# Kernel tuning notes

Measured on AMD Instinct MI355X. Metric: run time of the kernel, lower is better.

## Reference

```python
import jax, jax.numpy as jnp
import numpy as np

D = 200      # embedding_dim
R = 460      # 2 * num_rel
T = 32       # num_t (timestamps)
B = 2048     # batch of queries
NUM_E = 10000


def _gru(x, h, W_ih, W_hh, b_ih, b_hh):
    # torch.nn.GRUCell semantics
    gi = x @ W_ih.T + b_ih
    gh = h @ W_hh.T + b_hh
    ir, iz, inn = jnp.split(gi, 3, axis=-1)
    hr, hz, hn = jnp.split(gh, 3, axis=-1)
    r = jax.nn.sigmoid(ir + hr)
    z = jax.nn.sigmoid(iz + hz)
    n = jnp.tanh(inn + r * hn)
    return (1.0 - z) * n + z * h


def _mk_linear(k, out_dim, in_dim):
    kw, kb = jax.random.split(k)
    bound = 1.0 / np.sqrt(in_dim)
    W = jax.random.uniform(kw, (out_dim, in_dim), minval=-bound, maxval=bound, dtype=jnp.float32)
    b = jax.random.uniform(kb, (out_dim,), minval=-bound, maxval=bound, dtype=jnp.float32)
    return W, b


def setup_inputs():
    key = jax.random.key(0)
    ks = jax.random.split(key, 20)
    pre_emb = jax.random.normal(ks[0], (NUM_E, D), dtype=jnp.float32) * 0.05
    r_emb = jax.random.normal(ks[1], (R, D), dtype=jnp.float32) * 0.05
    sub = jax.random.randint(ks[2], (B,), 0, NUM_E)
    rel = jax.random.randint(ks[3], (B,), 0, R)
    obj = jax.random.randint(ks[4], (B,), 0, NUM_E)
    all_triples = jnp.stack([sub, rel, obj], axis=1)
    mask = jax.random.bernoulli(ks[5], 0.1, (B, T * R))
    partial_embeding = jax.random.uniform(ks[6], (B, T * R), dtype=jnp.float32) * mask
    cur_ts = jax.random.randint(ks[7], (B,), 0, T)
    W_map1, b_map1 = _mk_linear(ks[8], 2 * D, D)
    W_map2, b_map2 = _mk_linear(ks[9], D, 2 * D)
    W_attn, b_attn = _mk_linear(ks[10], D, D)
    W_ih, b_ih = _mk_linear(ks[11], 3 * D, D)
    W_hh, b_hh = _mk_linear(ks[12], 3 * D, D)
    W_h1, b_h1 = _mk_linear(ks[13], D, D)
    W_h2, b_h2 = _mk_linear(ks[14], D, D)
    W_align, b_align = _mk_linear(ks[15], D, D)
    return {
        'pre_emb': pre_emb, 'r_emb': r_emb, 'all_triples': all_triples,
        'partial_embeding': partial_embeding, 'cur_ts': cur_ts,
        'W_map1': W_map1, 'b_map1': b_map1, 'W_map2': W_map2, 'b_map2': b_map2,
        'W_attn': W_attn, 'b_attn': b_attn,
        'W_ih': W_ih, 'W_hh': W_hh, 'b_ih': b_ih, 'b_hh': b_hh,
        'W_h1': W_h1, 'b_h1': b_h1, 'W_h2': W_h2, 'b_h2': b_h2,
        'W_align': W_align, 'b_align': b_align,
    }


def reference(pre_emb, r_emb, all_triples, partial_embeding, cur_ts,
              W_map1, b_map1, W_map2, b_map2, W_attn, b_attn,
              W_ih, W_hh, b_ih, b_hh, W_h1, b_h1, W_h2, b_h2,
              W_align, b_align):
    # rel_mapping2(rel_mapping1(r_emb)) -> [R, D]
    mapped_rel = (r_emb @ W_map1.T + b_map1) @ W_map2.T + b_map2
    q_rel = mapped_rel[all_triples[:, 1]]                      # [B, D]
    # attention logits base is constant over timesteps: linear_attn(q_rel) @ mapped_rel^T
    base = (q_rel @ W_attn.T + b_attn) @ mapped_rel.T          # [B, R]
    part = partial_embeding.reshape(B, T, R).transpose(1, 0, 2)  # [T, B, R]
    ts = jnp.arange(T)

    # The torch code sorts by cur_ts and runs GRU steps for ts in [0, cur_ts_j) per sample.
    # Equivalent fully-batched form: scan over T, freeze hidden once t >= cur_ts_j.
    def step(h, inp):
        t, cur = inp                                           # cur: [B, R]
        attn = cur * base
        attn = jnp.where(attn == 0, jnp.float32(-1e9), attn)
        a = jax.nn.softmax(attn, axis=1)
        x = a @ mapped_rel                                     # [B, D]
        h_new = _gru(x, h, W_ih, W_hh, b_ih, b_hh)
        h = jnp.where((t < cur_ts)[:, None], h_new, h)
        return h, None

    h0 = jnp.zeros((B, D), dtype=jnp.float32)
    gru_hidden_all, _ = jax.lax.scan(step, h0, (ts, part))

    # predicted_hist = 0.1 * rel2hist2(rel2hist(q_rel)) + q_rel
    predicted_hist = 0.1 * ((q_rel @ W_h1.T + b_h1) @ W_h2.T + b_h2) + q_rel
    match_loss = jnp.mean((predicted_hist - gru_hidden_all) ** 2)

    # forward_forth with distmult scoring
    gh = _gru(q_rel, predicted_hist, W_ih, W_hh, b_ih, b_hh)
    sub_emb = pre_emb[all_triples[:, 0]]
    aligned_all = pre_emb @ W_align.T + b_align                # [NUM_E, D]
    aligned_sub = sub_emb @ W_align.T + b_align                # [B, D]
    score_ = (aligned_sub * gh) @ aligned_all.T                # [B, NUM_E]
    labels = jax.nn.one_hot(all_triples[:, 2], NUM_E, dtype=jnp.float32)
    # BCELoss(sigmoid(score_), labels), stably via log-sigmoid
    path_loss = -jnp.mean(labels * jax.nn.log_sigmoid(score_)
                          + (1.0 - labels) * jax.nn.log_sigmoid(-score_))
    score = jax.nn.sigmoid(score_)
    return match_loss, path_loss, score
```

## Files before the change

### kernel.cpp

```cpp
#include <hip/hip_runtime.h>
#include <cstdint>
#include <cstddef>

typedef unsigned short u16;
typedef __attribute__((ext_vector_type(8))) short short8;
typedef __attribute__((ext_vector_type(4))) float f32x4;

__device__ __forceinline__ f32x4 mfma16(short8 a, short8 b, f32x4 c){
  return __builtin_amdgcn_mfma_f32_16x16x32_bf16(a, b, c, 0, 0, 0);
}
__device__ __forceinline__ float bf2f(u16 u){
  unsigned v = ((unsigned)u) << 16; float f; __builtin_memcpy(&f, &v, 4); return f;
}
__device__ __forceinline__ u16 f2bf(float f){
  unsigned u; __builtin_memcpy(&u, &f, 4);
  u += 0x7FFFu + ((u >> 16) & 1u);
  return (u16)(u >> 16);
}
__device__ __forceinline__ float sigf(float x){ return 1.f / (1.f + __expf(-x)); }

struct CvtD { const float* s; u16* d; int M, K, Mp, Kp; };
struct CvtTab { CvtD t[10]; };

__global__ void cvt_all(CvtTab tab){
  CvtD de = tab.t[blockIdx.y];
  int total = de.Mp * de.Kp;
  for (int i = blockIdx.x * blockDim.x + threadIdx.x; i < total; i += gridDim.x * blockDim.x){
    int r = i / de.Kp, c = i - r * de.Kp;
    float v = (r < de.M && c < de.K) ? de.s[(size_t)r * de.K + c] : 0.f;
    de.d[i] = f2bf(v);
  }
}

__global__ void gather_qrel(const u16* __restrict__ mbf, const float* __restrict__ m32,
                            const int* __restrict__ trip, u16* __restrict__ qbf,
                            float* __restrict__ q32){
  int i = blockIdx.x * blockDim.x + threadIdx.x;
  if (i < 2048 * 256){
    int b = i >> 8, c = i & 255;
    int rel = trip[b * 3 + 1];
    qbf[i] = mbf[rel * 256 + c];
    if (c < 200) q32[b * 200 + c] = m32[rel * 200 + c];
  }
}

__global__ void cntt_k(const int* __restrict__ cur_ts, int* __restrict__ cntt,
                       float* __restrict__ out0){
  int t = blockIdx.x;
  __shared__ int psum[256];
  int tid = threadIdx.x, s = 0;
  #pragma unroll
  for (int k = 0; k < 8; ++k) s += (cur_ts[tid * 8 + k] > t) ? 1 : 0;
  psum[tid] = s; __syncthreads();
  for (int st = 128; st > 0; st >>= 1){
    if (tid < st) psum[tid] += psum[tid + st];
    __syncthreads();
  }
  if (tid == 0){
    cntt[t] = psum[0];
    if (t == 0){ out0[0] = 0.f; out0[1] = 0.f; }
  }
}
__global__ void toff_k(const int* __restrict__ cntt, int* __restrict__ toff){
  if (threadIdx.x == 0){
    int run = 0;
    for (int t = 0; t < 32; ++t){ toff[t] = run; run += cntt[t]; }
    toff[32] = run;
  }
}
__global__ void fill_pairs_t(const int* __restrict__ cur_ts, const int* __restrict__ toff,
                             int* __restrict__ pairs){
  int t = blockIdx.x;
  __shared__ int psum[256];
  int tid = threadIdx.x;
  int loc[8]; int tsum = 0;
  #pragma unroll
  for (int k = 0; k < 8; ++k){ loc[k] = (cur_ts[tid * 8 + k] > t) ? 1 : 0; tsum += loc[k]; }
  psum[tid] = tsum; __syncthreads();
  for (int st = 1; st < 256; st <<= 1){
    int v = (tid >= st) ? psum[tid - st] : 0;
    __syncthreads();
    psum[tid] += v;
    __syncthreads();
  }
  int run = psum[tid] - tsum + toff[t];
  #pragma unroll
  for (int k = 0; k < 8; ++k)
    if (loc[k]){ pairs[run] = t * 2048 + tid * 8 + k; ++run; }
}

template<int MODE, int GROUP>
__global__ __launch_bounds__(256) void gemm_bt(
    const u16* A, int lda,
    const u16* B, int ldb,
    int K, int Mreal, int Nreal,
    const float* bias,
    float* C32,
    u16* C16, int ldc16,
    const float* __restrict__ extra,
    const float* __restrict__ extra2,
    const int* __restrict__ trip,
    float* __restrict__ loss,
    const int* __restrict__ tcnt,
    const u16* A2, const u16* B2, const float* bias2, float* C32b, u16* C16b,
    int Mreal2, int ldc16b)
{
  __shared__ u16 AB[3][2][128 * 32];
  __shared__ float red[256];
  const int tid = threadIdx.x;
  const int wave = tid >> 6, lane = tid & 63;

  if (MODE == 0 && blockIdx.z){
    A = A2; B = B2; bias = bias2; C32 = C32b; C16 = C16b;
    Mreal = Mreal2; ldc16 = ldc16b;
  }

  const int gx = gridDim.x, gy = gridDim.y;
  const int nwg = gx * gy;
  int orig = blockIdx.y * gx + blockIdx.x;
  int q = nwg >> 3, r8 = nwg & 7;
  int xcd = orig & 7, idx = orig >> 3;
  int fid = (xcd < r8 ? xcd * (q + 1) : r8 * (q + 1) + (xcd - r8) * q) + idx;
  int mx, my;
  if (GROUP == 0){ my = fid / gx; mx = fid - my * gx; }
  else           { mx = fid / gy; my = fid - mx * gy; }

  const int m0 = my * 128, n0 = mx * 128;

  int Mg_ = Mreal;
  if (MODE == 3) Mg_ = tcnt[32];
  if (m0 >= Mg_) return;

  const int wm = (wave >> 1) * 64, wn = (wave & 1) * 64;
  const int srow = lane >> 2;
  const int scol = (((lane & 3) ^ (srow & 3)) * 8);
  const int fr = lane & 15, fkg = lane >> 4;
  const int slot = (fkg ^ (fr & 3)) * 8;

  f32x4 acc[4][4];
  #pragma unroll
  for (int i = 0; i < 4; ++i)
    #pragma unroll
    for (int j = 0; j < 4; ++j) acc[i][j] = (f32x4){0.f, 0.f, 0.f, 0.f};

  const int kT = (K + 31) >> 5;

  auto STAGE = [&](int kt, int p){
    #pragma unroll
    for (int i = 0; i < 2; ++i){
      int ch = wave * 2 + i;
      const u16* ga = A + (size_t)(m0 + ch * 16 + srow) * lda + kt * 32 + scol;
      __builtin_amdgcn_global_load_lds((const __attribute__((address_space(1))) void*)ga,
          (__attribute__((address_space(3))) void*)(&AB[p][0][0] + ch * 512), 16, 0, 0);
      const u16* gb = B + (size_t)(n0 + ch * 16 + srow) * ldb + kt * 32 + scol;
      __builtin_amdgcn_global_load_lds((const __attribute__((address_space(1))) void*)gb,
          (__attribute__((address_space(3))) void*)(&AB[p][1][0] + ch * 512), 16, 0, 0);
    }
  };

  STAGE(0, 0);
  if (kT > 1) STAGE(1, 1);
  for (int kt = 0; kt < kT; ++kt){
    const int p = kt % 3;
    if (kt + 1 < kT){
      __builtin_amdgcn_sched_barrier(0);
      asm volatile("s_waitcnt vmcnt(4)" ::: "memory");
    } else {
      __builtin_amdgcn_sched_barrier(0);
      asm volatile("s_waitcnt vmcnt(0)" ::: "memory");
    }
    __builtin_amdgcn_sched_barrier(0);
    __builtin_amdgcn_s_barrier();
    __builtin_amdgcn_sched_barrier(0);

    if (kt + 2 < kT) STAGE(kt + 2, (kt + 2) % 3);

    short8 av[4], bv[4];
    #pragma unroll
    for (int i = 0; i < 4; ++i){
      av[i] = *(const short8*)(&AB[p][0][0] + (wm + i * 16 + fr) * 32 + slot);
      bv[i] = *(const short8*)(&AB[p][1][0] + (wn + i * 16 + fr) * 32 + slot);
    }
    #pragma unroll
    for (int i = 0; i < 4; ++i)
      #pragma unroll
      for (int j = 0; j < 4; ++j)
        acc[i][j] = mfma16(av[i], bv[j], acc[i][j]);
  }

  if (MODE == 2){
    float lsum = 0.f;
    #pragma unroll
    for (int i = 0; i < 4; ++i){
      #pragma unroll
      for (int r = 0; r < 4; ++r){
        int row = m0 + wm + i * 16 + (lane >> 4) * 4 + r;
        int tcol = trip[row * 3 + 2];
        #pragma unroll
        for (int j = 0; j < 4; ++j){
          int col = n0 + wn + j * 16 + fr;
          if (col < Nreal){
            float v = acc[i][j][r];
            float e = __expf(-fabsf(v));
            float inv = __builtin_amdgcn_rcpf(1.f + e);
            C32[2 + (size_t)row * Nreal + col] = (v >= 0.f) ? inv : e * inv;
            float x = (tcol == col) ? v : -v;
            lsum += fminf(x, 0.f) - __logf(1.f + e);
          }
        }
      }
    }
    red[tid] = lsum;
    __syncthreads();
    for (int s = 128; s > 0; s >>= 1){
      if (tid < s) red[tid] += red[tid + s];
      __syncthreads();
    }
    if (tid == 0) atomicAdd(loss, -red[0] * (1.f / 20480000.f));
    return;
  }

  if (MODE == 3){
    #pragma unroll
    for (int i = 0; i < 4; ++i){
      #pragma unroll
      for (int r = 0; r < 4; ++r){
        int row = m0 + wm + i * 16 + (lane >> 4) * 4 + r;
        if (row < Mg_){
          int orow = trip[row];
          #pragma unroll
          for (int j = 0; j < 4; ++j){
            int col = n0 + wn + j * 16 + fr;
            if (col < Nreal)
              C16[(size_t)orow * ldc16 + col] = f2bf(acc[i][j][r] + bias[col]);
          }
        }
      }
    }
    return;
  }

  if (MODE == 1){
    float lsum = 0.f;
    #pragma unroll
    for (int i = 0; i < 4; ++i){
      #pragma unroll
      for (int j = 0; j < 4; ++j){
        int col = n0 + wn + j * 16 + fr;
        float bvl = (col < Nreal) ? bias[col] : 0.f;
        #pragma unroll
        for (int r = 0; r < 4; ++r){
          int row = m0 + wm + i * 16 + (lane >> 4) * 4 + r;
          if (col < Nreal){
            float pv = 0.1f * (acc[i][j][r] + bvl) + extra[(size_t)row * Nreal + col];
            C32[(size_t)row * Nreal + col] = pv;
            C16[(size_t)row * ldc16 + col] = f2bf(pv);
            float d = pv - extra2[(size_t)row * Nreal + col];
            lsum += d * d;
          } else {
            C16[(size_t)row * ldc16 + col] = 0;
          }
        }
      }
    }
    red[tid] = lsum;
    __syncthreads();
    for (int s = 128; s > 0; s >>= 1){
      if (tid < s) red[tid] += red[tid + s];
      __syncthreads();
    }
    if (tid == 0) atomicAdd(loss, red[0] * (1.f / 409600.f));
    return;
  }

  #pragma unroll
  for (int i = 0; i < 4; ++i){
    #pragma unroll
    for (int j = 0; j < 4; ++j){
      int col = n0 + wn + j * 16 + fr;
      float bvl = 0.f;
      if (bias && col < Nreal) bvl = bias[col];
      #pragma unroll
      for (int r = 0; r < 4; ++r){
        int row = m0 + wm + i * 16 + (lane >> 4) * 4 + r;
        float v = acc[i][j][r] + bvl;
        if (C32 && row < Mreal && col < Nreal) C32[(size_t)row * Nreal + col] = v;
        if (C16) C16[(size_t)row * ldc16 + col] =
            (row < Mreal && col < Nreal) ? f2bf(v) : (u16)0;
      }
    }
  }
}

__global__ __launch_bounds__(256) void softmax_c(
    const float* __restrict__ part, const float* __restrict__ base,
    const int* __restrict__ pairs, const int* __restrict__ toff,
    u16* __restrict__ aout)
{
  int wave = threadIdx.x >> 6, lane = threadIdx.x & 63;
  int hi = toff[32];
  for (int j = blockIdx.x * 4 + wave; j < hi; j += gridDim.x * 4){
    int p = pairs[j];
    int b = p & 2047, t = p >> 11;
    const float* pr = part + (size_t)b * 14720 + t * 460;
    const float* br = base + (size_t)b * 460;
    int r0 = lane * 8;
    float vals[8];
    if (lane < 57){
      float4 pa = *(const float4*)(pr + r0);
      float4 pb = *(const float4*)(pr + r0 + 4);
      float4 ba = *(const float4*)(br + r0);
      float4 bb = *(const float4*)(br + r0 + 4);
      float pv[8] = {pa.x, pa.y, pa.z, pa.w, pb.x, pb.y, pb.z, pb.w};
      float bw[8] = {ba.x, ba.y, ba.z, ba.w, bb.x, bb.y, bb.z, bb.w};
      #pragma unroll
      for (int u = 0; u < 8; ++u){
        float a = pv[u] * bw[u];
        bool valid = (r0 + u) < 460;
        vals[u] = (!valid) ? -__builtin_inff() : ((a == 0.f) ? -1000000000.0f : a);
      }
    } else {
      #pragma unroll
      for (int u = 0; u < 8; ++u){
        int r = r0 + u;
        if (r < 460){
          float a = pr[r] * br[r];
          vals[u] = (a == 0.f) ? -1000000000.0f : a;
        } else vals[u] = -__builtin_inff();
      }
    }
    float m = vals[0];
    #pragma unroll
    for (int u = 1; u < 8; ++u) m = fmaxf(m, vals[u]);
    #pragma unroll
    for (int s = 1; s < 64; s <<= 1) m = fmaxf(m, __shfl_xor(m, s));
    float e[8]; float sum = 0.f;
    #pragma unroll
    for (int u = 0; u < 8; ++u){
      float x = vals[u];
      float ev = (x == -__builtin_inff()) ? 0.f : __expf(x - m);
      e[u] = ev; sum += ev;
    }
    #pragma unroll
    for (int s = 1; s < 64; s <<= 1) sum += __shfl_xor(sum, s);
    float inv = __builtin_amdgcn_rcpf(sum);
    union { u16 o[8]; uint4 v; } pk;
    #pragma unroll
    for (int u = 0; u < 8; ++u) pk.o[u] = f2bf(e[u] * inv);
    *(uint4*)(aout + (size_t)j * 512 + r0) = pk.v;
  }
}

__global__ __launch_bounds__(512, 2) void gru_scan3(
    const u16* __restrict__ gi_all,
    const u16* __restrict__ Whh,
    const float* __restrict__ bhh,
    const int* __restrict__ cur_ts,
    float* __restrict__ hout)
{
  __shared__ u16 hbf[16 * 256];
  __shared__ float hf[8 * 200];
  __shared__ float ghs[8][648];
  __shared__ u16 gis[2][8 * 640];
  __shared__ float bhs[600];
  __shared__ int cts[8];
  const int tid = threadIdx.x, wave = tid >> 6, lane = tid & 63;
  const int rb = blockIdx.x * 8;
  const int fr = lane & 15, fkg = lane >> 4;
  const int fk = fkg * 8;

  for (int i = tid; i < 16 * 256; i += 512) hbf[i] = 0;
  for (int i = tid; i < 8 * 200; i += 512) hf[i] = 0.f;
  for (int i = tid; i < 600; i += 512) bhs[i] = bhh[i];
  if (tid < 8) cts[tid] = cur_ts[rb + tid];
  __syncthreads();
  int Trun = 0;
  #pragma unroll
  for (int r = 0; r < 8; ++r) Trun = max(Trun, cts[r]);

  short8 wb[5][7];
  #pragma unroll
  for (int f = 0; f < 5; ++f)
    #pragma unroll
    for (int ks = 0; ks < 7; ++ks)
      wb[f][ks] = *(const short8*)(Whh + (size_t)(wave * 80 + f * 16 + fr) * 256 + ks * 32 + fk);

  if (Trun > 0){
    const u16* src = gi_all + (size_t)rb * 640;
    __builtin_amdgcn_global_load_lds(
        (const __attribute__((address_space(1))) void*)(src + tid * 8),
        (__attribute__((address_space(3))) void*)(&gis[0][0] + tid * 8), 16, 0, 0);
    if (tid < 128)
      __builtin_amdgcn_global_load_lds(
          (const __attribute__((address_space(1))) void*)(src + (512 + tid) * 8),
          (__attribute__((address_space(3))) void*)(&gis[0][0] + (512 + tid) * 8), 16, 0, 0);
  }
  __syncthreads();

  const int grow = wave;
  const int crow = (Trun > 0) ? cts[grow] : 0;

  for (int t = 0; t < Trun; ++t){
    f32x4 acc[5];
    #pragma unroll
    for (int f = 0; f < 5; ++f) acc[f] = (f32x4){0.f, 0.f, 0.f, 0.f};
    #pragma unroll
    for (int ks = 0; ks < 7; ++ks){
      short8 av = *(const short8*)(hbf + ((fr * 256 + ks * 32 + fk) ^ ((fr & 7) << 3)));
      #pragma unroll
      for (int f = 0; f < 5; ++f)
        acc[f] = mfma16(av, wb[f][ks], acc[f]);
    }
    if (fkg < 2){
      #pragma unroll
      for (int f = 0; f < 5; ++f){
        int col = wave * 80 + f * 16 + fr;
        #pragma unroll
        for (int r = 0; r < 4; ++r)
          ghs[fkg * 4 + r][col] = acc[f][r];
      }
    }
    __builtin_amdgcn_sched_barrier(0);
    asm volatile("s_waitcnt vmcnt(0) lgkmcnt(0)" ::: "memory");
    __builtin_amdgcn_sched_barrier(0);
    __builtin_amdgcn_s_barrier();
    __builtin_amdgcn_sched_barrier(0);

    if (t + 1 < Trun){
      const u16* src = gi_all + ((size_t)(t + 1) * 2048 + rb) * 640;
      u16* dst = &gis[(t + 1) & 1][0];
      __builtin_amdgcn_global_load_lds(
          (const __attribute__((address_space(1))) void*)(src + tid * 8),
          (__attribute__((address_space(3))) void*)(dst + tid * 8), 16, 0, 0);
      if (tid < 128)
        __builtin_amdgcn_global_load_lds(
            (const __attribute__((address_space(1))) void*)(src + (512 + tid) * 8),
            (__attribute__((address_space(3))) void*)(dst + (512 + tid) * 8), 16, 0, 0);
    }

    if (t < crow){
      const u16* gr = &gis[t & 1][0] + grow * 640;
      #pragma unroll
      for (int k = 0; k < 4; ++k){
        int d = lane + 64 * k;
        if (d < 200){
          float i0 = bf2f(gr[d]);
          float i1 = bf2f(gr[200 + d]);
          float i2 = bf2f(gr[400 + d]);
          float g0 = ghs[grow][d] + bhs[d];
          float g1 = ghs[grow][200 + d] + bhs[200 + d];
          float g2 = ghs[grow][400 + d] + bhs[400 + d];
          float e0 = __expf(-(i0 + g0));
          float r_ = __builtin_amdgcn_rcpf(1.f + e0);
          float e1 = __expf(-(i1 + g1));
          float z  = __builtin_amdgcn_rcpf(1.f + e1);
          float xn = i2 + r_ * g2;
          float e2 = __expf(2.f * xn);
          float n_ = 1.f - 2.f * __builtin_amdgcn_rcpf(e2 + 1.f);
          float hn = (1.f - z) * n_ + z * hf[grow * 200 + d];
          hf[grow * 200 + d] = hn;
          hbf[(grow * 256 + d) ^ (grow << 3)] = f2bf(hn);
        }
      }
    }
    __builtin_amdgcn_sched_barrier(0);
    asm volatile("s_waitcnt lgkmcnt(0)" ::: "memory");
    __builtin_amdgcn_sched_barrier(0);
    __builtin_amdgcn_s_barrier();
    __builtin_amdgcn_sched_barrier(0);
  }

  for (int i = tid; i < 1600; i += 512){
    int row = i / 200, d = i - row * 200;
    hout[(size_t)(rb + row) * 200 + d] = hf[row * 200 + d];
  }
}

__global__ __launch_bounds__(256) void gru2_abig(const float* __restrict__ gi,
                                                 const float* __restrict__ gg,
                                                 const float* __restrict__ hprev,
                                                 const float* __restrict__ al32,
                                                 const int* __restrict__ trip,
                                                 u16* __restrict__ abig){
  int i = blockIdx.x * 256 + threadIdx.x;
  if (i < 2048 * 256){
    int b = i >> 8, c = i & 255;
    u16 v = 0;
    if (c < 200){
      float i0 = gi[b * 600 + c], i1 = gi[b * 600 + 200 + c], i2 = gi[b * 600 + 400 + c];
      float g0 = gg[b * 600 + c], g1 = gg[b * 600 + 200 + c], g2 = gg[b * 600 + 400 + c];
      float r = sigf(i0 + g0);
      float z = sigf(i1 + g1);
      float n = tanhf(i2 + r * g2);
      float gh = (1.f - z) * n + z * hprev[b * 200 + c];
      int sub = trip[b * 3 + 0];
      v = f2bf(al32[(size_t)sub * 200 + c] * gh);
    }
    abig[i] = v;
  }
}

extern "C" void kernel_launch(void* const* d_in, const int* in_sizes, int n_in,
                              void* d_out, int out_size, void* d_ws, size_t ws_size,
                              hipStream_t stream)
{
  (void)in_sizes; (void)n_in; (void)out_size; (void)ws_size;
  const float* pre_emb = (const float*)d_in[0];
  const float* r_emb   = (const float*)d_in[1];
  const int*   trip    = (const int*)d_in[2];
  const float* part    = (const float*)d_in[3];
  const int*   cur_ts  = (const int*)d_in[4];
  const float* Wmap1 = (const float*)d_in[5];   const float* bmap1 = (const float*)d_in[6];
  const float* Wmap2 = (const float*)d_in[7];   const float* bmap2 = (const float*)d_in[8];
  const float* Wattn = (const float*)d_in[9];   const float* battn = (const float*)d_in[10];
  const float* Wih   = (const float*)d_in[11];  const float* Whh   = (const float*)d_in[12];
  const float* bih   = (const float*)d_in[13];  const float* bhh   = (const float*)d_in[14];
  const float* Wh1   = (const float*)d_in[15];  const float* bh1   = (const float*)d_in[16];
  const float* Wh2   = (const float*)d_in[17];  const float* bh2   = (const float*)d_in[18];
  const float* Wal   = (const float*)d_in[19];  const float* bal   = (const float*)d_in[20];
  float* out = (float*)d_out;

  char* wsb = (char*)d_ws;
  size_t off = 0;
  auto alloc = [&](size_t bytes) -> void* {
    void* p = wsb + off;
    off = (off + bytes + 255) & ~(size_t)255;
    return p;
  };
  u16* re_bf     = (u16*)alloc((size_t)512 * 256 * 2);
  u16* wmap1_bf  = (u16*)alloc((size_t)512 * 256 * 2);
  u16* wmap2_bf  = (u16*)alloc((size_t)256 * 448 * 2);
  u16* wattn_bf  = (u16*)alloc((size_t)256 * 256 * 2);
  u16* wih_bf    = (u16*)alloc((size_t)640 * 256 * 2);
  u16* whh_bf    = (u16*)alloc((size_t)640 * 256 * 2);
  u16* wh1_bf    = (u16*)alloc((size_t)256 * 256 * 2);
  u16* wh2_bf    = (u16*)alloc((size_t)256 * 256 * 2);
  u16* wal_bf    = (u16*)alloc((size_t)256 * 256 * 2);
  u16* pre_bf    = (u16*)alloc((size_t)10112 * 256 * 2);
  u16* hidden_bf = (u16*)alloc((size_t)512 * 512 * 2);
  u16* mrel_bf   = (u16*)alloc((size_t)512 * 256 * 2);
  u16* m2t_bf    = (u16*)alloc((size_t)640 * 512 * 2);
  u16* qrel_bf   = (u16*)alloc((size_t)2048 * 256 * 2);
  u16* qa_bf     = (u16*)alloc((size_t)2048 * 256 * 2);
  u16* ph1_bf    = (u16*)alloc((size_t)2048 * 256 * 2);
  u16* ph_bf     = (u16*)alloc((size_t)2048 * 256 * 2);
  u16* abig_bf   = (u16*)alloc((size_t)2048 * 256 * 2);
  u16* gi_all    = (u16*)alloc((size_t)65536 * 640 * 2);
  float* mrel32 = (float*)alloc((size_t)460 * 200 * 4);
  float* base32 = (float*)alloc((size_t)2048 * 460 * 4);
  float* qrel32 = (float*)alloc((size_t)2048 * 200 * 4);
  float* hout   = (float*)alloc((size_t)2048 * 200 * 4);
  float* ph32   = (float*)alloc((size_t)2048 * 200 * 4);
  int* pairs    = (int*)alloc((size_t)65536 * 4);
  int* cntt     = (int*)alloc((size_t)64 * 4);
  int* toff     = (int*)alloc((size_t)64 * 4);
  char* U = (char*)alloc((size_t)40000 * 512 * 2);
  u16*   a_comp = (u16*)U;
  float* gi2    = (float*)(U);
  float* ghg    = (float*)(U + (size_t)5  * 1024 * 1024);
  float* al32   = (float*)(U + (size_t)12 * 1024 * 1024);
  u16*   al_bf  = (u16*)  (U + (size_t)21 * 1024 * 1024);

  cntt_k<<<32, 256, 0, stream>>>(cur_ts, cntt, out);
  toff_k<<<1, 32, 0, stream>>>(cntt, toff);
  fill_pairs_t<<<32, 256, 0, stream>>>(cur_ts, toff, pairs);

  CvtTab tab;
  tab.t[0] = { r_emb,   re_bf,    460, 200,   512, 256 };
  tab.t[1] = { Wmap1,   wmap1_bf, 400, 200,   512, 256 };
  tab.t[2] = { Wmap2,   wmap2_bf, 200, 400,   256, 448 };
  tab.t[3] = { Wattn,   wattn_bf, 200, 200,   256, 256 };
  tab.t[4] = { Wih,     wih_bf,   600, 200,   640, 256 };
  tab.t[5] = { Whh,     whh_bf,   600, 200,   640, 256 };
  tab.t[6] = { Wh1,     wh1_bf,   200, 200,   256, 256 };
  tab.t[7] = { Wh2,     wh2_bf,   200, 200,   256, 256 };
  tab.t[8] = { Wal,     wal_bf,   200, 200,   256, 256 };
  tab.t[9] = { pre_emb, pre_bf, 10000, 200, 10112, 256 };
  cvt_all<<<dim3(512, 10), 256, 0, stream>>>(tab);

  gemm_bt<0,0><<<dim3(4, 4), 256, 0, stream>>>(re_bf, 256, wmap1_bf, 256, 200, 460, 400,
      bmap1, nullptr, hidden_bf, 512, nullptr, nullptr, nullptr, nullptr, nullptr,
      nullptr, nullptr, nullptr, nullptr, nullptr, 0, 0);
  gemm_bt<0,0><<<dim3(2, 4), 256, 0, stream>>>(hidden_bf, 512, wmap2_bf, 448, 400, 460, 200,
      bmap2, mrel32, mrel_bf, 256, nullptr, nullptr, nullptr, nullptr, nullptr,
      nullptr, nullptr, nullptr, nullptr, nullptr, 0, 0);
  gather_qrel<<<2048, 256, 0, stream>>>(mrel_bf, mrel32, trip, qrel_bf, qrel32);

  gemm_bt<0,0><<<dim3(2, 16, 2), 256, 0, stream>>>(qrel_bf, 256, wattn_bf, 256, 200, 2048, 200,
      battn, nullptr, qa_bf, 256, nullptr, nullptr, nullptr, nullptr, nullptr,
      qrel_bf, wh1_bf, bh1, nullptr, ph1_bf, 2048, 256);

  gemm_bt<0,0><<<dim3(4, 16, 2), 256, 0, stream>>>(qa_bf, 256, mrel_bf, 256, 200, 2048, 460,
      nullptr, base32, nullptr, 0, nullptr, nullptr, nullptr, nullptr, nullptr,
      wih_bf, mrel_bf, nullptr, nullptr, m2t_bf, 600, 512);

  softmax_c<<<2048, 256, 0, stream>>>(part, base32, pairs, toff, a_comp);
  gemm_bt<3,0><<<dim3(5, 313), 256, 0, stream>>>(a_comp, 512, m2t_bf, 512, 460, 0, 600,
      bih, nullptr, gi_all, 640, nullptr, nullptr, pairs, nullptr, toff,
      nullptr, nullptr, nullptr, nullptr, nullptr, 0, 0);

  gru_scan3<<<256, 512, 0, stream>>>(gi_all, whh_bf, bhh, cur_ts, hout);

  gemm_bt<1,0><<<dim3(2, 16), 256, 0, stream>>>(ph1_bf, 256, wh2_bf, 256, 200, 2048, 200,
      bh2, ph32, ph_bf, 256, qrel32, hout, nullptr, out, nullptr,
      nullptr, nullptr, nullptr, nullptr, nullptr, 0, 0);

  gemm_bt<0,0><<<dim3(5, 16, 2), 256, 0, stream>>>(qrel_bf, 256, wih_bf, 256, 200, 2048, 600,
      bih, gi2, nullptr, 0, nullptr, nullptr, nullptr, nullptr, nullptr,
      ph_bf, whh_bf, bhh, ghg, nullptr, 2048, 0);

  gemm_bt<0,0><<<dim3(2, 79), 256, 0, stream>>>(pre_bf, 256, wal_bf, 256, 200, 10000, 200,
      bal, al32, al_bf, 256, nullptr, nullptr, nullptr, nullptr, nullptr,
      nullptr, nullptr, nullptr, nullptr, nullptr, 0, 0);

  gru2_abig<<<2048, 256, 0, stream>>>(gi2, ghg, ph32, al32, trip, abig_bf);

  gemm_bt<2,1><<<dim3(79, 16), 256, 0, stream>>>(abig_bf, 256, al_bf, 256, 200, 2048, 10000,
      nullptr, out, nullptr, 0, nullptr, nullptr, trip, out + 1, nullptr,
      nullptr, nullptr, nullptr, nullptr, nullptr, 0, 0);
}
```

Before: 341.2 us.

## Replace LDS-staged GEMM pipeline with direct global fragment loads and compile-time K

The GEMM kernel no longer stages A/B tiles through shared memory with a triple-buffered global_load_lds pipeline and barriers. Each wave now loads its MFMA fragments straight from global memory, and the K-tile count becomes a template parameter so the loop fully unrolls. This removes barrier and LDS traffic for these small-K GEMMs, but each wave re-reads data that other waves also fetch and relies on cache for reuse. The scratch buffer is enlarged slightly, likely to cover reads past row ends.

```diff
diff --git a/kernel.cpp b/kernel.cpp
--- a/kernel.cpp
+++ b/kernel.cpp
@@ -89,7 +89,7 @@
     if (loc[k]){ pairs[run] = t * 2048 + tid * 8 + k; ++run; }
 }
 
-template<int MODE, int GROUP>
+template<int MODE, int GROUP, int KT>
 __global__ __launch_bounds__(256) void gemm_bt(
     const u16* A, int lda,
     const u16* B, int ldb,
@@ -105,7 +105,6 @@
     const u16* A2, const u16* B2, const float* bias2, float* C32b, u16* C16b,
     int Mreal2, int ldc16b)
 {
-  __shared__ u16 AB[3][2][128 * 32];
   __shared__ float red[256];
   const int tid = threadIdx.x;
   const int wave = tid >> 6, lane = tid & 63;
@@ -132,10 +131,10 @@
   if (m0 >= Mg_) return;
 
   const int wm = (wave >> 1) * 64, wn = (wave & 1) * 64;
-  const int srow = lane >> 2;
-  const int scol = (((lane & 3) ^ (srow & 3)) * 8);
   const int fr = lane & 15, fkg = lane >> 4;
-  const int slot = (fkg ^ (fr & 3)) * 8;
+
+  const u16* Ab = A + (size_t)(m0 + wm + fr) * lda + fkg * 8;
+  const u16* Bb = B + (size_t)(n0 + wn + fr) * ldb + fkg * 8;
 
   f32x4 acc[4][4];
   #pragma unroll
@@ -143,43 +142,13 @@
     #pragma unroll
     for (int j = 0; j < 4; ++j) acc[i][j] = (f32x4){0.f, 0.f, 0.f, 0.f};
 
-  const int kT = (K + 31) >> 5;
-
-  auto STAGE = [&](int kt, int p){
-    #pragma unroll
-    for (int i = 0; i < 2; ++i){
-      int ch = wave * 2 + i;
-      const u16* ga = A + (size_t)(m0 + ch * 16 + srow) * lda + kt * 32 + scol;
-      __builtin_amdgcn_global_load_lds((const __attribute__((address_space(1))) void*)ga,
-          (__attribute__((address_space(3))) void*)(&AB[p][0][0] + ch * 512), 16, 0, 0);
-      const u16* gb = B + (size_t)(n0 + ch * 16 + srow) * ldb + kt * 32 + scol;
-      __builtin_amdgcn_global_load_lds((const __attribute__((address_space(1))) void*)gb,
-          (__attribute__((address_space(3))) void*)(&AB[p][1][0] + ch * 512), 16, 0, 0);
-    }
-  };
-
-  STAGE(0, 0);
-  if (kT > 1) STAGE(1, 1);
-  for (int kt = 0; kt < kT; ++kt){
-    const int p = kt % 3;
-    if (kt + 1 < kT){
-      __builtin_amdgcn_sched_barrier(0);
-      asm volatile("s_waitcnt vmcnt(4)" ::: "memory");
-    } else {
-      __builtin_amdgcn_sched_barrier(0);
-      asm volatile("s_waitcnt vmcnt(0)" ::: "memory");
-    }
-    __builtin_amdgcn_sched_barrier(0);
-    __builtin_amdgcn_s_barrier();
-    __builtin_amdgcn_sched_barrier(0);
-
-    if (kt + 2 < kT) STAGE(kt + 2, (kt + 2) % 3);
-
+  #pragma unroll
+  for (int kt = 0; kt < KT; ++kt){
     short8 av[4], bv[4];
     #pragma unroll
     for (int i = 0; i < 4; ++i){
-      av[i] = *(const short8*)(&AB[p][0][0] + (wm + i * 16 + fr) * 32 + slot);
-      bv[i] = *(const short8*)(&AB[p][1][0] + (wn + i * 16 + fr) * 32 + slot);
+      av[i] = *(const short8*)(Ab + (size_t)(i * 16) * lda + kt * 32);
+      bv[i] = *(const short8*)(Bb + (size_t)(i * 16) * ldb + kt * 32);
     }
     #pragma unroll
     for (int i = 0; i < 4; ++i)
@@ -554,7 +523,7 @@
   int* pairs    = (int*)alloc((size_t)65536 * 4);
   int* cntt     = (int*)alloc((size_t)64 * 4);
   int* toff     = (int*)alloc((size_t)64 * 4);
-  char* U = (char*)alloc((size_t)40000 * 512 * 2);
+  char* U = (char*)alloc((size_t)40200 * 512 * 2);
   u16*   a_comp = (u16*)U;
   float* gi2    = (float*)(U);
   float* ghg    = (float*)(U + (size_t)5  * 1024 * 1024);
@@ -578,44 +547,44 @@
   tab.t[9] = { pre_emb, pre_bf, 10000, 200, 10112, 256 };
   cvt_all<<<dim3(512, 10), 256, 0, stream>>>(tab);
 
-  gemm_bt<0,0><<<dim3(4, 4), 256, 0, stream>>>(re_bf, 256, wmap1_bf, 256, 200, 460, 400,
+  gemm_bt<0,0,7><<<dim3(4, 4), 256, 0, stream>>>(re_bf, 256, wmap1_bf, 256, 200, 460, 400,
       bmap1, nullptr, hidden_bf, 512, nullptr, nullptr, nullptr, nullptr, nullptr,
       nullptr, nullptr, nullptr, nullptr, nullptr, 0, 0);
-  gemm_bt<0,0><<<dim3(2, 4), 256, 0, stream>>>(hidden_bf, 512, wmap2_bf, 448, 400, 460, 200,
+  gemm_bt<0,0,13><<<dim3(2, 4), 256, 0, stream>>>(hidden_bf, 512, wmap2_bf, 448, 400, 460, 200,
       bmap2, mrel32, mrel_bf, 256, nullptr, nullptr, nullptr, nullptr, nullptr,
       nullptr, nullptr, nullptr, nullptr, nullptr, 0, 0);
   gather_qrel<<<2048, 256, 0, stream>>>(mrel_bf, mrel32, trip, qrel_bf, qrel32);
 
-  gemm_bt<0,0><<<dim3(2, 16, 2), 256, 0, stream>>>(qrel_bf, 256, wattn_bf, 256, 200, 2048, 200,
+  gemm_bt<0,0,7><<<dim3(2, 16, 2), 256, 0, stream>>>(qrel_bf, 256, wattn_bf, 256, 200, 2048, 200,
       battn, nullptr, qa_bf, 256, nullptr, nullptr, nullptr, nullptr, nullptr,
       qrel_bf, wh1_bf, bh1, nullptr, ph1_bf, 2048, 256);
 
-  gemm_bt<0,0><<<dim3(4, 16, 2), 256, 0, stream>>>(qa_bf, 256, mrel_bf, 256, 200, 2048, 460,
+  gemm_bt<0,0,7><<<dim3(4, 16, 2), 256, 0, stream>>>(qa_bf, 256, mrel_bf, 256, 200, 2048, 460,
       nullptr, base32, nullptr, 0, nullptr, nullptr, nullptr, nullptr, nullptr,
       wih_bf, mrel_bf, nullptr, nullptr, m2t_bf, 600, 512);
 
   softmax_c<<<2048, 256, 0, stream>>>(part, base32, pairs, toff, a_comp);
-  gemm_bt<3,0><<<dim3(5, 313), 256, 0, stream>>>(a_comp, 512, m2t_bf, 512, 460, 0, 600,
+  gemm_bt<3,0,15><<<dim3(5, 313), 256, 0, stream>>>(a_comp, 512, m2t_bf, 512, 460, 0, 600,
       bih, nullptr, gi_all, 640, nullptr, nullptr, pairs, nullptr, toff,
       nullptr, nullptr, nullptr, nullptr, nullptr, 0, 0);
 
   gru_scan3<<<256, 512, 0, stream>>>(gi_all, whh_bf, bhh, cur_ts, hout);
 
-  gemm_bt<1,0><<<dim3(2, 16), 256, 0, stream>>>(ph1_bf, 256, wh2_bf, 256, 200, 2048, 200,
+  gemm_bt<1,0,7><<<dim3(2, 16), 256, 0, stream>>>(ph1_bf, 256, wh2_bf, 256, 200, 2048, 200,
       bh2, ph32, ph_bf, 256, qrel32, hout, nullptr, out, nullptr,
       nullptr, nullptr, nullptr, nullptr, nullptr, 0, 0);
 
-  gemm_bt<0,0><<<dim3(5, 16, 2), 256, 0, stream>>>(qrel_bf, 256, wih_bf, 256, 200, 2048, 600,
+  gemm_bt<0,0,7><<<dim3(5, 16, 2), 256, 0, stream>>>(qrel_bf, 256, wih_bf, 256, 200, 2048, 600,
       bih, gi2, nullptr, 0, nullptr, nullptr, nullptr, nullptr, nullptr,
       ph_bf, whh_bf, bhh, ghg, nullptr, 2048, 0);
 
-  gemm_bt<0,0><<<dim3(2, 79), 256, 0, stream>>>(pre_bf, 256, wal_bf, 256, 200, 10000, 200,
+  gemm_bt<0,0,7><<<dim3(2, 79), 256, 0, stream>>>(pre_bf, 256, wal_bf, 256, 200, 10000, 200,
       bal, al32, al_bf, 256, nullptr, nullptr, nullptr, nullptr, nullptr,
       nullptr, nullptr, nullptr, nullptr, nullptr, 0, 0);
 
   gru2_abig<<<2048, 256, 0, stream>>>(gi2, ghg, ph32, al32, trip, abig_bf);
 
-  gemm_bt<2,1><<<dim3(79, 16), 256, 0, stream>>>(abig_bf, 256, al_bf, 256, 200, 2048, 10000,
+  gemm_bt<2,1,7><<<dim3(79, 16), 256, 0, stream>>>(abig_bf, 256, al_bf, 256, 200, 2048, 10000,
       nullptr, out, nullptr, 0, nullptr, nullptr, trip, out + 1, nullptr,
       nullptr, nullptr, nullptr, nullptr, nullptr, 0, 0);
 }
```

New measurement: 471.3 us. 38.1% more time.
